# Optimization experiments

Hardware: AMD Instinct MI355X
Metric: run time of the kernel (lower is better)

The kernel has to match this reference:

```python
import jax, jax.numpy as jnp
import numpy as np

N_NODES = 50000
N_EDGES = 1600000
NODE_DIM = 64
HIDDEN_DIM = 128
EDGE_DIM = 32


def _linear_params(key, fan_in, fan_out, bias=True):
    k1, k2 = jax.random.split(key)
    bound = 1.0 / np.sqrt(fan_in)
    W = jax.random.uniform(k1, (fan_in, fan_out), minval=-bound, maxval=bound, dtype=jnp.float32)
    if bias:
        b = jax.random.uniform(k2, (fan_out,), minval=-bound, maxval=bound, dtype=jnp.float32)
        return W, b
    return W, None


def setup_inputs() -> dict:
    key = jax.random.key(0)
    ks = jax.random.split(key, 12)
    h = jax.random.normal(ks[0], (N_NODES, NODE_DIM), dtype=jnp.float32)
    x = jax.random.normal(ks[1], (N_NODES, 3), dtype=jnp.float32) * 10.0
    edge_index = jax.random.randint(ks[2], (2, N_EDGES), 0, N_NODES, dtype=jnp.int32).astype(jnp.int64)
    edge_dist = jax.random.uniform(ks[3], (N_EDGES,), dtype=jnp.float32) * 10.0

    msg_in = 2 * NODE_DIM + EDGE_DIM
    node_w1, node_b1 = _linear_params(ks[4], msg_in, HIDDEN_DIM)
    node_w2, node_b2 = _linear_params(ks[5], HIDDEN_DIM, NODE_DIM)
    coord_w1, coord_b1 = _linear_params(ks[6], msg_in, HIDDEN_DIM)
    coord_w2, _ = _linear_params(ks[7], HIDDEN_DIM, 1, bias=False)
    edge_w1, edge_b1 = _linear_params(ks[8], 1, EDGE_DIM)
    edge_w2, edge_b2 = _linear_params(ks[9], EDGE_DIM, EDGE_DIM)

    return dict(h=h, x=x, edge_index=edge_index, edge_dist=edge_dist,
                node_w1=node_w1, node_b1=node_b1, node_w2=node_w2, node_b2=node_b2,
                coord_w1=coord_w1, coord_b1=coord_b1, coord_w2=coord_w2,
                edge_w1=edge_w1, edge_b1=edge_b1, edge_w2=edge_w2, edge_b2=edge_b2)


def reference(h, x, edge_index, edge_dist,
              node_w1, node_b1, node_w2, node_b2,
              coord_w1, coord_b1, coord_w2,
              edge_w1, edge_b1, edge_w2, edge_b2):
    src = edge_index[0]
    dst = edge_index[1]

    # edge_mlp: Linear(1, edge_dim) -> SiLU -> Linear(edge_dim, edge_dim)
    edge_attr = jax.nn.silu(edge_dist[:, None] @ edge_w1 + edge_b1) @ edge_w2 + edge_b2

    # per-edge message input: [E, 2*node_dim + edge_dim]
    m_input = jnp.concatenate([h[src], h[dst], edge_attr], axis=-1)

    # node_mlp: Linear -> SiLU -> Linear
    m = jax.nn.silu(m_input @ node_w1 + node_b1) @ node_w2 + node_b2
    h_agg = jnp.zeros_like(h).at[dst].add(m)

    # coord_mlp: Linear -> SiLU -> Linear(hidden, 1, bias=False)
    coord_weight = jax.nn.silu(m_input @ coord_w1 + coord_b1) @ coord_w2  # [E, 1]

    dir_vec = x[src] - x[dst]                               # [E, 3]
    dir_len = jnp.maximum(jnp.linalg.norm(dir_vec, axis=-1, keepdims=True), 1e-8)
    coord_update = coord_weight * (dir_vec / dir_len)
    x_agg = jnp.zeros_like(x).at[dst].add(coord_update)

    return (h + h_agg, x + x_agg)
```

## Files before the change

### kernel.cpp

```cpp
#include <hip/hip_runtime.h>
#include <hip/hip_bf16.h>
#include <stdint.h>

#define NN 50000
#define NE 1600000
#define BE 128

typedef __attribute__((ext_vector_type(8))) short short8;
typedef __attribute__((ext_vector_type(4))) float f32x4;

__device__ __forceinline__ unsigned short f2bf(float f) {
    unsigned int u = __float_as_uint(f);
    u += 0x7fff + ((u >> 16) & 1);
    return (unsigned short)(u >> 16);
}

__device__ __forceinline__ unsigned int pk2bf(float lo, float hi) {
    __hip_bfloat162 b = __float22bfloat162_rn(float2{lo, hi});
    return *(unsigned int*)&b;
}

__device__ __forceinline__ float silu_f(float v) {
    return v * __builtin_amdgcn_rcpf(1.0f + __expf(-v));
}

__global__ void prep_kernel(const float* __restrict__ nw1,
                            const float* __restrict__ cw1,
                            const float* __restrict__ nw2,
                            unsigned short* __restrict__ ws) {
    int i = blockIdx.x * 256 + threadIdx.x;
    if (i < 20480) {
        int n = i / 160, k = i % 160;
        ws[i] = f2bf(nw1[k * 128 + n]);
    } else if (i < 40960) {
        int j = i - 20480; int n = j / 160, k = j % 160;
        ws[i] = f2bf(cw1[k * 128 + n]);
    } else if (i < 49152) {
        int j = i - 40960; int o = j / 128, k = j % 128;
        ws[i] = f2bf(nw2[k * 64 + o]);
    }
}

__global__ void init_out(const float4* __restrict__ h4,
                         const float4* __restrict__ x4,
                         float4* __restrict__ out4) {
    int i = blockIdx.x * 256 + threadIdx.x;
    if (i < 800000)       out4[i] = h4[i];
    else if (i < 837500)  out4[i] = x4[i - 800000];
}

#define MIS 168

__global__ __launch_bounds__(256, 3)
void egnn_edge_kernel(const float* __restrict__ h,
                      const float* __restrict__ x,
                      const int* __restrict__ eidx,
                      const float* __restrict__ edist,
                      const float* __restrict__ node_b1,
                      const float* __restrict__ node_b2,
                      const float* __restrict__ coord_b1,
                      const float* __restrict__ coord_w2,
                      const float* __restrict__ ew1,
                      const float* __restrict__ eb1,
                      const float* __restrict__ ew2,
                      const float* __restrict__ eb2,
                      const unsigned short* __restrict__ ws,
                      float* __restrict__ out_h,
                      float* __restrict__ out_x) {
    __shared__ unsigned short mi[BE * MIS];
    __shared__ int srcS[BE];
    __shared__ int dstS[BE];

    const int tid  = threadIdx.x;
    const int w    = tid >> 6;
    const int lane = tid & 63;
    const int ln   = lane & 15;
    const int quad = lane >> 4;
    const int e0   = blockIdx.x * BE;

    if (tid < BE)      srcS[tid]       = eidx[e0 + tid];
    else               dstS[tid - BE]  = eidx[NE + e0 + tid - BE];
    __syncthreads();

    {
        const float4* h4 = (const float4*)h;
        const int g = tid >> 4, l16 = tid & 15;
        #pragma unroll
        for (int it = 0; it < 16; ++it) {
            int row = it * 16 + g;
            int e = row & 127;
            int node = (row < 128) ? srcS[e] : dstS[e];
            int cbase = (row < 128) ? 0 : 64;
            float4 v = h4[node * 16 + l16];
            uint2 u;
            u.x = pk2bf(v.x, v.y);
            u.y = pk2bf(v.z, v.w);
            *(uint2*)&mi[e * MIS + cbase + l16 * 4] = u;
        }
    }
    {
        int e = tid >> 1, half = tid & 1;
        float d = edist[e0 + e];
        float s[16];
        #pragma unroll
        for (int jj = 0; jj < 16; ++jj) s[jj] = eb2[half * 16 + jj];
        #pragma unroll
        for (int k = 0; k < 32; ++k) {
            float tk = silu_f(d * ew1[k] + eb1[k]);
            const float* r2 = ew2 + k * 32 + half * 16;
            #pragma unroll
            for (int jj = 0; jj < 16; ++jj) s[jj] += tk * r2[jj];
        }
        uint4 u0, u1;
        u0.x = pk2bf(s[0], s[1]);  u0.y = pk2bf(s[2], s[3]);
        u0.z = pk2bf(s[4], s[5]);  u0.w = pk2bf(s[6], s[7]);
        u1.x = pk2bf(s[8], s[9]);  u1.y = pk2bf(s[10], s[11]);
        u1.z = pk2bf(s[12], s[13]); u1.w = pk2bf(s[14], s[15]);
        *(uint4*)&mi[e * MIS + 128 + half * 16]     = u0;
        *(uint4*)&mi[e * MIS + 128 + half * 16 + 8] = u1;
    }

    __syncthreads();

    const int arow0 = (w * 32 + ln) * MIS;
    const int arow1 = (w * 32 + 16 + ln) * MIS;
    const int koff  = quad * 8;
    const f32x4 zero = {0.f, 0.f, 0.f, 0.f};

    short8 aA[5], aB[5];
    #pragma unroll
    for (int kc = 0; kc < 5; ++kc) {
        aA[kc] = *(const short8*)&mi[arow0 + kc * 32 + koff];
        aB[kc] = *(const short8*)&mi[arow1 + kc * 32 + koff];
    }

    const int wvoff = ln * 160 + koff;

    f32x4 accC[2][8];
    #pragma unroll
    for (int a = 0; a < 2; ++a)
        #pragma unroll
        for (int b = 0; b < 8; ++b) accC[a][b] = zero;
    {
        const unsigned short* wsrc = ws + 20480;
        #pragma unroll
        for (int half = 0; half < 2; ++half) {
            #pragma unroll
            for (int kc = 0; kc < 5; ++kc) {
                #pragma unroll
                for (int nt = 0; nt < 4; ++nt) {
                    short8 b = *(const short8*)(wsrc + half * 10240 + nt * 2560
                                                + kc * 32 + wvoff);
                    const int nn = half * 4 + nt;
                    accC[0][nn] = __builtin_amdgcn_mfma_f32_16x16x32_bf16(aA[kc], b, accC[0][nn], 0, 0, 0);
                    accC[1][nn] = __builtin_amdgcn_mfma_f32_16x16x32_bf16(aB[kc], b, accC[1][nn], 0, 0, 0);
                }
            }
        }
    }

    {
        float cw[2][4];
        #pragma unroll
        for (int mt = 0; mt < 2; ++mt)
            #pragma unroll
            for (int r = 0; r < 4; ++r) cw[mt][r] = 0.f;
        #pragma unroll
        for (int nt = 0; nt < 8; ++nt) {
            int col = nt * 16 + ln;
            float b1v = coord_b1[col];
            float w2v = coord_w2[col];
            #pragma unroll
            for (int mt = 0; mt < 2; ++mt)
                #pragma unroll
                for (int r = 0; r < 4; ++r)
                    cw[mt][r] += silu_f(accC[mt][nt][r] + b1v) * w2v;
        }
        #pragma unroll
        for (int off = 1; off < 16; off <<= 1) {
            #pragma unroll
            for (int mt = 0; mt < 2; ++mt)
                #pragma unroll
                for (int r = 0; r < 4; ++r)
                    cw[mt][r] += __shfl_xor(cw[mt][r], off, 64);
        }
        if (ln < 8) {
            const int smt = ln >> 2, sr = ln & 3;
            float cwsel = 0.f;
            #pragma unroll
            for (int mt = 0; mt < 2; ++mt)
                #pragma unroll
                for (int r = 0; r < 4; ++r)
                    cwsel = (mt == smt && r == sr) ? cw[mt][r] : cwsel;
            int lrow = w * 32 + smt * 16 + quad * 4 + sr;
            int s = srcS[lrow], dn = dstS[lrow];
            float dx = x[s * 3]     - x[dn * 3];
            float dy = x[s * 3 + 1] - x[dn * 3 + 1];
            float dz = x[s * 3 + 2] - x[dn * 3 + 2];
            float len = fmaxf(sqrtf(dx * dx + dy * dy + dz * dz), 1e-8f);
            float k = cwsel * __builtin_amdgcn_rcpf(len);
            atomicAdd(out_x + dn * 3,     k * dx);
            atomicAdd(out_x + dn * 3 + 1, k * dy);
            atomicAdd(out_x + dn * 3 + 2, k * dz);
        }
    }

    f32x4 accN[2][8];
    #pragma unroll
    for (int a = 0; a < 2; ++a)
        #pragma unroll
        for (int b = 0; b < 8; ++b) accN[a][b] = zero;
    {
        const unsigned short* wsrc = ws;
        #pragma unroll
        for (int half = 0; half < 2; ++half) {
            #pragma unroll
            for (int kc = 0; kc < 5; ++kc) {
                #pragma unroll
                for (int nt = 0; nt < 4; ++nt) {
                    short8 b = *(const short8*)(wsrc + half * 10240 + nt * 2560
                                                + kc * 32 + wvoff);
                    const int nn = half * 4 + nt;
                    accN[0][nn] = __builtin_amdgcn_mfma_f32_16x16x32_bf16(aA[kc], b, accN[0][nn], 0, 0, 0);
                    accN[1][nn] = __builtin_amdgcn_mfma_f32_16x16x32_bf16(aB[kc], b, accN[1][nn], 0, 0, 0);
                }
            }
        }
    }

    #pragma unroll
    for (int mt = 0; mt < 2; ++mt) {
        const int rowb = (w * 32 + mt * 16 + quad * 4) * MIS;
        #pragma unroll
        for (int nt = 0; nt < 8; ++nt) {
            int col = nt * 16 + ln;
            float b1v = node_b1[col];
            #pragma unroll
            for (int r = 0; r < 4; ++r)
                mi[rowb + r * MIS + col] = f2bf(silu_f(accN[mt][nt][r] + b1v));
        }
    }

    f32x4 acc2[2][4];
    #pragma unroll
    for (int a = 0; a < 2; ++a)
        #pragma unroll
        for (int b = 0; b < 4; ++b) acc2[a][b] = zero;
    const unsigned short* nw2T = ws + 40960;
    #pragma unroll
    for (int kc = 0; kc < 4; ++kc) {
        short8 a0 = *(const short8*)&mi[arow0 + kc * 32 + koff];
        short8 a1 = *(const short8*)&mi[arow1 + kc * 32 + koff];
        #pragma unroll
        for (int nt = 0; nt < 4; ++nt) {
            short8 b = *(const short8*)(nw2T + (nt * 16 + ln) * 128 + kc * 32 + koff);
            acc2[0][nt] = __builtin_amdgcn_mfma_f32_16x16x32_bf16(a0, b, acc2[0][nt], 0, 0, 0);
            acc2[1][nt] = __builtin_amdgcn_mfma_f32_16x16x32_bf16(a1, b, acc2[1][nt], 0, 0, 0);
        }
    }
    #pragma unroll
    for (int mt = 0; mt < 2; ++mt) {
        #pragma unroll
        for (int r = 0; r < 4; ++r) {
            int lrow = w * 32 + mt * 16 + quad * 4 + r;
            int dn = dstS[lrow];
            float* outrow = out_h + (size_t)dn * 64;
            #pragma unroll
            for (int nt = 0; nt < 4; ++nt) {
                int col = nt * 16 + ln;
                atomicAdd(outrow + col, acc2[mt][nt][r] + node_b2[col]);
            }
        }
    }
}

extern "C" void kernel_launch(void* const* d_in, const int* in_sizes, int n_in,
                              void* d_out, int out_size, void* d_ws, size_t ws_size,
                              hipStream_t stream) {
    const float* h    = (const float*)d_in[0];
    const float* x    = (const float*)d_in[1];
    const int*   eidx = (const int*)d_in[2];
    const float* edist= (const float*)d_in[3];
    const float* nw1  = (const float*)d_in[4];
    const float* nb1  = (const float*)d_in[5];
    const float* nw2  = (const float*)d_in[6];
    const float* nb2  = (const float*)d_in[7];
    const float* cw1  = (const float*)d_in[8];
    const float* cb1  = (const float*)d_in[9];
    const float* cw2  = (const float*)d_in[10];
    const float* ew1  = (const float*)d_in[11];
    const float* eb1  = (const float*)d_in[12];
    const float* ew2  = (const float*)d_in[13];
    const float* eb2  = (const float*)d_in[14];
    float* out = (float*)d_out;
    unsigned short* ws = (unsigned short*)d_ws;

    prep_kernel<<<192, 256, 0, stream>>>(nw1, cw1, nw2, ws);
    init_out<<<3272, 256, 0, stream>>>((const float4*)h, (const float4*)x, (float4*)out);
    egnn_edge_kernel<<<NE / BE, 256, 0, stream>>>(h, x, eidx, edist,
                                                  nb1, nb2, cb1, cw2,
                                                  ew1, eb1, ew2, eb2,
                                                  ws, out, out + 3200000);
}
```

Measured before the change: 828.6 us.

## Pre-convert node features to bf16, pack coords, and run edge MLP on MFMA

Adds a pre-pass that converts h to bf16 once in workspace, so each edge gather reads half the bytes and skips the per-edge conversion. It also packs x into float4 so each coordinate fetch is a single aligned load. The second edge-MLP layer moves from scalar FMAs to a small bf16 MFMA against a transposed ew2 staged in workspace. Both fast paths depend on the workspace being large enough and add extra small kernels; the MFMA path also adds rounding of the edge-MLP hidden activations to bf16.

New measurement: 742.3 us. -10.4%, faster.

```diff
diff --git a/kernel.cpp b/kernel.cpp
--- a/kernel.cpp
+++ b/kernel.cpp
@@ -24,9 +24,16 @@
     return v * __builtin_amdgcn_rcpf(1.0f + __expf(-v));
 }
 
+#define WS_EW2T_US   49152
+#define WS_HB_B      100352
+#define WS_XP_B      6500352
+#define WS_HB_NEED   6500352
+#define WS_XP_NEED   7300352
+
 __global__ void prep_kernel(const float* __restrict__ nw1,
                             const float* __restrict__ cw1,
                             const float* __restrict__ nw2,
+                            const float* __restrict__ ew2,
                             unsigned short* __restrict__ ws) {
     int i = blockIdx.x * 256 + threadIdx.x;
     if (i < 20480) {
@@ -38,6 +45,29 @@
     } else if (i < 49152) {
         int j = i - 40960; int o = j / 128, k = j % 128;
         ws[i] = f2bf(nw2[k * 64 + o]);
+    } else if (i < 50176) {
+        int j = i - 49152; int jo = j >> 5, k = j & 31;
+        ws[i] = f2bf(ew2[k * 32 + jo]);
+    }
+}
+
+__global__ void hcvt_kernel(const float4* __restrict__ h4,
+                            unsigned short* __restrict__ hb) {
+    int i = blockIdx.x * 256 + threadIdx.x;
+    if (i < 800000) {
+        float4 v = h4[i];
+        uint2 u;
+        u.x = pk2bf(v.x, v.y);
+        u.y = pk2bf(v.z, v.w);
+        *(uint2*)&hb[i * 4] = u;
+    }
+}
+
+__global__ void xpack_kernel(const float* __restrict__ x,
+                             float4* __restrict__ xp) {
+    int n = blockIdx.x * 256 + threadIdx.x;
+    if (n < NN) {
+        xp[n] = float4{x[n * 3], x[n * 3 + 1], x[n * 3 + 2], 0.f};
     }
 }
 
@@ -53,7 +83,9 @@
 
 __global__ __launch_bounds__(256, 3)
 void egnn_edge_kernel(const float* __restrict__ h,
+                      const unsigned short* __restrict__ hb,
                       const float* __restrict__ x,
+                      const float4* __restrict__ xp,
                       const int* __restrict__ eidx,
                       const float* __restrict__ edist,
                       const float* __restrict__ node_b1,
@@ -62,7 +94,6 @@
                       const float* __restrict__ coord_w2,
                       const float* __restrict__ ew1,
                       const float* __restrict__ eb1,
-                      const float* __restrict__ ew2,
                       const float* __restrict__ eb2,
                       const unsigned short* __restrict__ ws,
                       float* __restrict__ out_h,
@@ -82,7 +113,18 @@
     else               dstS[tid - BE]  = eidx[NE + e0 + tid - BE];
     __syncthreads();
 
-    {
+    if (hb) {
+        const uint2* hb2 = (const uint2*)hb;
+        const int g = tid >> 4, l16 = tid & 15;
+        #pragma unroll
+        for (int it = 0; it < 16; ++it) {
+            int row = it * 16 + g;
+            int e = row & 127;
+            int node = (row < 128) ? srcS[e] : dstS[e];
+            int cbase = (row < 128) ? 0 : 64;
+            *(uint2*)&mi[e * MIS + cbase + l16 * 4] = hb2[node * 16 + l16];
+        }
+    } else {
         const float4* h4 = (const float4*)h;
         const int g = tid >> 4, l16 = tid & 15;
         #pragma unroll
@@ -101,21 +143,17 @@
     {
         int e = tid >> 1, half = tid & 1;
         float d = edist[e0 + e];
-        float s[16];
-        #pragma unroll
-        for (int jj = 0; jj < 16; ++jj) s[jj] = eb2[half * 16 + jj];
-        #pragma unroll
-        for (int k = 0; k < 32; ++k) {
-            float tk = silu_f(d * ew1[k] + eb1[k]);
-            const float* r2 = ew2 + k * 32 + half * 16;
-            #pragma unroll
-            for (int jj = 0; jj < 16; ++jj) s[jj] += tk * r2[jj];
+        float t[16];
+        #pragma unroll
+        for (int j = 0; j < 16; ++j) {
+            int k = half * 16 + j;
+            t[j] = silu_f(d * ew1[k] + eb1[k]);
         }
         uint4 u0, u1;
-        u0.x = pk2bf(s[0], s[1]);  u0.y = pk2bf(s[2], s[3]);
-        u0.z = pk2bf(s[4], s[5]);  u0.w = pk2bf(s[6], s[7]);
-        u1.x = pk2bf(s[8], s[9]);  u1.y = pk2bf(s[10], s[11]);
-        u1.z = pk2bf(s[12], s[13]); u1.w = pk2bf(s[14], s[15]);
+        u0.x = pk2bf(t[0], t[1]);   u0.y = pk2bf(t[2], t[3]);
+        u0.z = pk2bf(t[4], t[5]);   u0.w = pk2bf(t[6], t[7]);
+        u1.x = pk2bf(t[8], t[9]);   u1.y = pk2bf(t[10], t[11]);
+        u1.z = pk2bf(t[12], t[13]); u1.w = pk2bf(t[14], t[15]);
         *(uint4*)&mi[e * MIS + 128 + half * 16]     = u0;
         *(uint4*)&mi[e * MIS + 128 + half * 16 + 8] = u1;
     }
@@ -126,6 +164,32 @@
     const int arow1 = (w * 32 + 16 + ln) * MIS;
     const int koff  = quad * 8;
     const f32x4 zero = {0.f, 0.f, 0.f, 0.f};
+
+    {
+        const unsigned short* e2T = ws + WS_EW2T_US;
+        short8 ta0 = *(const short8*)&mi[arow0 + 128 + koff];
+        short8 ta1 = *(const short8*)&mi[arow1 + 128 + koff];
+        f32x4 ea[2][2];
+        ea[0][0] = zero; ea[0][1] = zero; ea[1][0] = zero; ea[1][1] = zero;
+        #pragma unroll
+        for (int nt = 0; nt < 2; ++nt) {
+            short8 b = *(const short8*)(e2T + (nt * 16 + ln) * 32 + koff);
+            ea[0][nt] = __builtin_amdgcn_mfma_f32_16x16x32_bf16(ta0, b, ea[0][nt], 0, 0, 0);
+            ea[1][nt] = __builtin_amdgcn_mfma_f32_16x16x32_bf16(ta1, b, ea[1][nt], 0, 0, 0);
+        }
+        #pragma unroll
+        for (int nt = 0; nt < 2; ++nt) {
+            int col = nt * 16 + ln;
+            float bv = eb2[col];
+            #pragma unroll
+            for (int rt = 0; rt < 2; ++rt) {
+                #pragma unroll
+                for (int r = 0; r < 4; ++r)
+                    mi[(w * 32 + rt * 16 + quad * 4 + r) * MIS + 128 + col] =
+                        f2bf(ea[rt][nt][r] + bv);
+            }
+        }
+    }
 
     short8 aA[5], aB[5];
     #pragma unroll
@@ -194,9 +258,15 @@
                     cwsel = (mt == smt && r == sr) ? cw[mt][r] : cwsel;
             int lrow = w * 32 + smt * 16 + quad * 4 + sr;
             int s = srcS[lrow], dn = dstS[lrow];
-            float dx = x[s * 3]     - x[dn * 3];
-            float dy = x[s * 3 + 1] - x[dn * 3 + 1];
-            float dz = x[s * 3 + 2] - x[dn * 3 + 2];
+            float dx, dy, dz;
+            if (xp) {
+                float4 xs = xp[s], xd = xp[dn];
+                dx = xs.x - xd.x; dy = xs.y - xd.y; dz = xs.z - xd.z;
+            } else {
+                dx = x[s * 3]     - x[dn * 3];
+                dy = x[s * 3 + 1] - x[dn * 3 + 1];
+                dz = x[s * 3 + 2] - x[dn * 3 + 2];
+            }
             float len = fmaxf(sqrtf(dx * dx + dy * dy + dz * dz), 1e-8f);
             float k = cwsel * __builtin_amdgcn_rcpf(len);
             atomicAdd(out_x + dn * 3,     k * dx);
@@ -295,10 +365,22 @@
     float* out = (float*)d_out;
     unsigned short* ws = (unsigned short*)d_ws;
 
-    prep_kernel<<<192, 256, 0, stream>>>(nw1, cw1, nw2, ws);
+    prep_kernel<<<196, 256, 0, stream>>>(nw1, cw1, nw2, ew2, ws);
     init_out<<<3272, 256, 0, stream>>>((const float4*)h, (const float4*)x, (float4*)out);
-    egnn_edge_kernel<<<NE / BE, 256, 0, stream>>>(h, x, eidx, edist,
+
+    unsigned short* hb = nullptr;
+    float4* xp = nullptr;
+    if (ws_size >= (size_t)WS_HB_NEED) {
+        hb = (unsigned short*)((char*)d_ws + WS_HB_B);
+        hcvt_kernel<<<3125, 256, 0, stream>>>((const float4*)h, hb);
+    }
+    if (ws_size >= (size_t)WS_XP_NEED) {
+        xp = (float4*)((char*)d_ws + WS_XP_B);
+        xpack_kernel<<<196, 256, 0, stream>>>(x, xp);
+    }
+
+    egnn_edge_kernel<<<NE / BE, 256, 0, stream>>>(h, hb, x, xp, eidx, edist,
                                                   nb1, nb2, cb1, cw2,
-                                                  ew1, eb1, ew2, eb2,
+                                                  ew1, eb1, eb2,
                                                   ws, out, out + 3200000);
 }
```
